# Optimization experiments

Measured on AMD Instinct MI355X. Metric: run time of the kernel, lower is better.

The kernel has to match this reference:

```python
import jax, jax.numpy as jnp
import numpy as np

N = 100000   # node_num
E = 1000000  # num edges
D = 256      # input_dim
H = 256      # hidden_dim


def setup_inputs() -> dict:
    key = jax.random.key(0)
    ks = jax.random.split(key, 6)
    x = jax.random.uniform(ks[0], (N, D), dtype=jnp.float32)  # nn.Parameter rand init
    edge_index = jax.random.randint(ks[1], (2, E), 0, N, dtype=jnp.int64)
    W1 = jax.random.normal(ks[2], (D, H), dtype=jnp.float32) * (1.0 / np.sqrt(D))
    b1 = jnp.zeros((H,), dtype=jnp.float32)
    W2 = jax.random.normal(ks[3], (H, H), dtype=jnp.float32) * (1.0 / np.sqrt(H))
    b2 = jnp.zeros((H,), dtype=jnp.float32)
    return {"edge_index": edge_index, "x": x, "W1": W1, "b1": b1, "W2": W2, "b2": b2}


def reference(edge_index, x, W1, b1, W2, b2):
    # GCNConv: add self-loops, symmetric normalization D^-1/2 (A+I) D^-1/2,
    # then (norm-weighted scatter-add of x@W) + bias, followed by ReLU.
    src, dst = edge_index[0], edge_index[1]
    loops = jnp.arange(N, dtype=src.dtype)
    s = jnp.concatenate([src, loops])          # [E+N] message sources
    d = jnp.concatenate([dst, loops])          # [E+N] message targets
    w = jnp.ones((E + N,), dtype=jnp.float32)  # edge_weight = 1 (incl. self-loops)
    deg = jax.ops.segment_sum(w, d, num_segments=N)
    dinv = jnp.where(deg > 0, jax.lax.rsqrt(deg), 0.0)
    norm = dinv[s] * w * dinv[d]               # [E+N]

    def layer(z, W, b):
        h = z @ W                                               # [N, H]
        agg = jax.ops.segment_sum(norm[:, None] * h[s], d, num_segments=N)
        return jax.nn.relu(agg + b)

    z = layer(x, W1, b1)
    z = layer(z, W2, b2)
    return z
```

## Files before the change

kernel.cpp:

```cpp
#include <hip/hip_runtime.h>
#include <stdint.h>

#define N_NODES 100000
#define N_EDGES 1000000
#define DIM 256
#define CAP 32

typedef __attribute__((ext_vector_type(8))) short short8;
typedef __attribute__((ext_vector_type(4))) float f32x4;
typedef __attribute__((ext_vector_type(4))) unsigned short u16x4;

__device__ inline float b2f(unsigned short u) {
    union { unsigned int i; float f; } v; v.i = ((unsigned int)u) << 16; return v.f;
}
__device__ inline unsigned short f2b(float f) {
    union { float f; unsigned int i; } v; v.f = f;
    unsigned int u = v.i;
    return (unsigned short)((u + 0x7FFFu + ((u >> 16) & 1u)) >> 16);
}


#define NB_FILL 245
#define NB_PACK 512
#define NB_CVT  25000

__global__ void k_pre(const int* __restrict__ src, const int* __restrict__ dst,
                      uint32_t* __restrict__ cnt, uint32_t* __restrict__ ovfCnt,
                      int* __restrict__ colM, uint32_t* __restrict__ ovf,
                      const float* __restrict__ W1, const float* __restrict__ W2,
                      unsigned short* __restrict__ Wt1, unsigned short* __restrict__ Wt2,
                      const float* __restrict__ x, unsigned short* __restrict__ xs) {
    int b = blockIdx.x, t = threadIdx.x;
    if (b < NB_FILL) {
        int e = b * 4096 + t;
        #pragma unroll
        for (int k = 0; k < 16; ++k, e += 256) {
            if (e < N_EDGES) {
                unsigned d = (unsigned)dst[e];
                unsigned s = (unsigned)src[e];
                if (d < N_NODES && s < N_NODES) {
                    uint32_t p = atomicAdd(&cnt[d], 1u);
                    if (p < CAP) colM[(size_t)d * CAP + p] = (int)s;
                    else {
                        uint32_t o = atomicAdd(ovfCnt, 1u);
                        if (o < (uint32_t)N_EDGES) { ovf[2 * o] = d; ovf[2 * o + 1] = s; }
                    }
                }
            }
        }
    } else if (b < NB_FILL + NB_PACK) {
        int n = b - NB_FILL;
        if (n < 256) Wt1[n * 256 + t] = f2b(W1[t * 256 + n]);
        else { n -= 256; Wt2[n * 256 + t] = f2b(W2[t * 256 + n]); }
    } else {
        int i = (b - (NB_FILL + NB_PACK)) * 256 + t;
        f32x4 v = __builtin_nontemporal_load((const f32x4*)x + i);
        u16x4 o;
        o.x = f2b(v.x); o.y = f2b(v.y); o.z = f2b(v.z); o.w = f2b(v.w);
        *((u16x4*)xs + i) = o;
    }
}

__global__ void k_wgt(const uint32_t* __restrict__ cnt, float* __restrict__ wgt) {
    int n = blockIdx.x * blockDim.x + threadIdx.x;
    if (n < N_NODES) wgt[n] = rsqrtf((float)(cnt[n] + 1u));
}

__global__ __launch_bounds__(256, 8) void k_gather(
        const unsigned short* __restrict__ rows, const uint32_t* __restrict__ cnt,
        const float* __restrict__ wgt,
        const uint32_t* __restrict__ ovfCnt, const int* __restrict__ colM,
        const uint32_t* __restrict__ ovf, unsigned short* __restrict__ out) {
    int wave = threadIdx.x >> 6, lane = threadIdx.x & 63;
    int node = blockIdx.x * 4 + wave;
    const u16x4* r4 = (const u16x4*)rows;

    uint32_t dgRaw = cnt[node];
    float    di    = wgt[node];
    uint32_t dg    = dgRaw < CAP ? dgRaw : CAP;
    uint32_t ovfN  = *ovfCnt;

    u16x4 sv = r4[(size_t)node * 64 + lane];
    float a[4];
    a[0] = di * b2f(sv.x); a[1] = di * b2f(sv.y);
    a[2] = di * b2f(sv.z); a[3] = di * b2f(sv.w);

    const int* cp = colM + (size_t)node * CAP;
    for (uint32_t j = 0; j < dg; j += 8) {
        int4 i0 = *(const int4*)(cp + j);
        int4 i1 = *(const int4*)(cp + j + 4);
        unsigned x0 = min((unsigned)i0.x, N_NODES - 1u);
        unsigned x1 = min((unsigned)i0.y, N_NODES - 1u);
        unsigned x2 = min((unsigned)i0.z, N_NODES - 1u);
        unsigned x3 = min((unsigned)i0.w, N_NODES - 1u);
        unsigned x4 = min((unsigned)i1.x, N_NODES - 1u);
        unsigned x5 = min((unsigned)i1.y, N_NODES - 1u);
        unsigned x6 = min((unsigned)i1.z, N_NODES - 1u);
        unsigned x7 = min((unsigned)i1.w, N_NODES - 1u);
        u16x4 r0 = r4[(size_t)x0 * 64 + lane];
        u16x4 r1 = r4[(size_t)x1 * 64 + lane];
        u16x4 r2 = r4[(size_t)x2 * 64 + lane];
        u16x4 r3 = r4[(size_t)x3 * 64 + lane];
        u16x4 r4v = r4[(size_t)x4 * 64 + lane];
        u16x4 r5 = r4[(size_t)x5 * 64 + lane];
        u16x4 r6 = r4[(size_t)x6 * 64 + lane];
        u16x4 r7 = r4[(size_t)x7 * 64 + lane];
        float w0 = (j + 0 < dg) ? wgt[x0] : 0.f;
        float w1 = (j + 1 < dg) ? wgt[x1] : 0.f;
        float w2 = (j + 2 < dg) ? wgt[x2] : 0.f;
        float w3 = (j + 3 < dg) ? wgt[x3] : 0.f;
        float w4 = (j + 4 < dg) ? wgt[x4] : 0.f;
        float w5 = (j + 5 < dg) ? wgt[x5] : 0.f;
        float w6 = (j + 6 < dg) ? wgt[x6] : 0.f;
        float w7 = (j + 7 < dg) ? wgt[x7] : 0.f;
        #pragma unroll
        for (int i = 0; i < 4; ++i) {
            float s = fmaf(w0, b2f(r0[i]), a[i]);
            s = fmaf(w1, b2f(r1[i]), s);
            s = fmaf(w2, b2f(r2[i]), s);
            s = fmaf(w3, b2f(r3[i]), s);
            s = fmaf(w4, b2f(r4v[i]), s);
            s = fmaf(w5, b2f(r5[i]), s);
            s = fmaf(w6, b2f(r6[i]), s);
            s = fmaf(w7, b2f(r7[i]), s);
            a[i] = s;
        }
    }

    if (ovfN) {
        for (uint32_t k = 0; k < ovfN; ++k) {
            uint32_t od = ovf[2 * k], os = ovf[2 * k + 1];
            if (od == (uint32_t)node) {
                float wv = wgt[os];
                u16x4 rv = r4[(size_t)os * 64 + lane];
                #pragma unroll
                for (int i = 0; i < 4; ++i) a[i] = fmaf(wv, b2f(rv[i]), a[i]);
            }
        }
    }

    u16x4 o;
    o.x = f2b(di * a[0]); o.y = f2b(di * a[1]);
    o.z = f2b(di * a[2]); o.w = f2b(di * a[3]);
    ((u16x4*)out)[(size_t)node * 64 + lane] = o;
}

__global__ __launch_bounds__(256, 4) void k_gemm(
        const unsigned short* __restrict__ A, const unsigned short* __restrict__ Wt,
        const float* __restrict__ bias,
        unsigned short* __restrict__ Cb, float* __restrict__ Cf) {
    __shared__ __align__(16) unsigned short As[64 * 256];

    int tid = threadIdx.x;
    int w = tid >> 6, lane = tid & 63;
    int rowBase = blockIdx.x * 64;

    #pragma unroll
    for (int i = 0; i < 8; ++i) {
        int c  = tid + i * 256;
        int r  = c >> 5;
        int kb = c & 31;
        int gr = rowBase + r;
        int4 v = {0, 0, 0, 0};
        if (gr < N_NODES) v = *(const int4*)(A + (size_t)gr * 256 + kb * 8);
        *(int4*)((char*)As + r * 512 + ((kb ^ (r & 7)) << 4)) = v;
    }
    __syncthreads();

    int m = lane & 15, quad = lane >> 4;

    f32x4 acc[4][4];
    #pragma unroll
    for (int mt = 0; mt < 4; ++mt)
        #pragma unroll
        for (int nt = 0; nt < 4; ++nt)
            acc[mt][nt] = (f32x4){0.f, 0.f, 0.f, 0.f};

    #pragma unroll
    for (int ks = 0; ks < 8; ++ks) {
        short8 wf[4], xf[4];
        #pragma unroll
        for (int nt = 0; nt < 4; ++nt)
            wf[nt] = *(const short8*)(Wt + (size_t)(w * 64 + nt * 16 + m) * 256 + ks * 32 + quad * 8);
        #pragma unroll
        for (int mt = 0; mt < 4; ++mt) {
            int rl = mt * 16 + m;
            int ch = (ks * 4 + quad) ^ (rl & 7);
            xf[mt] = *(const short8*)((const char*)As + rl * 512 + (ch << 4));
        }
        #pragma unroll
        for (int mt = 0; mt < 4; ++mt)
            #pragma unroll
            for (int nt = 0; nt < 4; ++nt)
                acc[mt][nt] = __builtin_amdgcn_mfma_f32_16x16x32_bf16(
                    wf[nt], xf[mt], acc[mt][nt], 0, 0, 0);
    }

    float4 bv[4];
    #pragma unroll
    for (int nt = 0; nt < 4; ++nt)
        bv[nt] = *(const float4*)(bias + w * 64 + nt * 16 + quad * 4);

    #pragma unroll
    for (int mt = 0; mt < 4; ++mt) {
        int node = rowBase + mt * 16 + m;
        if (node >= N_NODES) continue;
        if (Cf) {
            #pragma unroll
            for (int nt = 0; nt < 4; ++nt) {
                int c = w * 64 + nt * 16 + quad * 4;
                f32x4 v = acc[mt][nt];
                f32x4 o;
                o.x = fmaxf(v[0] + bv[nt].x, 0.f);
                o.y = fmaxf(v[1] + bv[nt].y, 0.f);
                o.z = fmaxf(v[2] + bv[nt].z, 0.f);
                o.w = fmaxf(v[3] + bv[nt].w, 0.f);
                __builtin_nontemporal_store(o, (f32x4*)(Cf + (size_t)node * 256 + c));
            }
        } else {
            #pragma unroll
            for (int nt = 0; nt < 4; ++nt) {
                int c = w * 64 + nt * 16 + quad * 4;
                f32x4 v = acc[mt][nt];
                u16x4 o;
                o.x = f2b(fmaxf(v[0] + bv[nt].x, 0.f));
                o.y = f2b(fmaxf(v[1] + bv[nt].y, 0.f));
                o.z = f2b(fmaxf(v[2] + bv[nt].z, 0.f));
                o.w = f2b(fmaxf(v[3] + bv[nt].w, 0.f));
                *(u16x4*)(Cb + (size_t)node * 256 + c) = o;
            }
        }
    }
}

extern "C" void kernel_launch(void* const* d_in, const int* in_sizes, int n_in,
                              void* d_out, int out_size, void* d_ws, size_t ws_size,
                              hipStream_t stream) {
    const int*   edge = (const int*)d_in[0];
    const float* x    = (const float*)d_in[1];
    const float* W1   = (const float*)d_in[2];
    const float* b1   = (const float*)d_in[3];
    const float* W2   = (const float*)d_in[4];
    const float* b2   = (const float*)d_in[5];
    float* out = (float*)d_out;

    char* ws = (char*)d_ws;
    uint32_t*       cnt    = (uint32_t*)(ws + 0);
    uint32_t*       ovfCnt = (uint32_t*)(ws + 400000);
    int*            colM   = (int*)     (ws + 400256);
    float*          wgt    = (float*)   (ws + 13200256);
    uint32_t*       ovf    = (uint32_t*)(ws + 13600256);
    unsigned short* Wt1    = (unsigned short*)(ws + 21600256);
    unsigned short* Wt2    = (unsigned short*)(ws + 21731328);
    unsigned short* xs     = (unsigned short*)(ws + 21862400);
    unsigned short* z1s    = (unsigned short*)(ws + 73062400ull);
    unsigned short* agg    = (unsigned short*)(ws + 124262400ull);

    const int* src = edge;
    const int* dst = edge + N_EDGES;

    hipMemsetAsync(ws, 0, 400256, stream);

    k_pre<<<NB_FILL + NB_PACK + NB_CVT, 256, 0, stream>>>(
        src, dst, cnt, ovfCnt, colM, ovf, W1, W2, Wt1, Wt2, x, xs);
    k_wgt<<<(N_NODES + 255) / 256, 256, 0, stream>>>(cnt, wgt);

    k_gather<<<N_NODES / 4, 256, 0, stream>>>(xs, cnt, wgt, ovfCnt, colM, ovf, agg);
    k_gemm<<<(N_NODES + 63) / 64, 256, 0, stream>>>(agg, Wt1, b1, z1s, nullptr);
    k_gather<<<N_NODES / 4, 256, 0, stream>>>(z1s, cnt, wgt, ovfCnt, colM, ovf, agg);
    k_gemm<<<(N_NODES + 63) / 64, 256, 0, stream>>>(agg, Wt2, b2, nullptr, out);
}
```

Before: 468.2 us.

## Fuse neighbor gather into GEMM kernel via shared-memory aggregation tile

```diff
diff --git a/kernel.cpp b/kernel.cpp
--- a/kernel.cpp
+++ b/kernel.cpp
@@ -66,87 +66,11 @@
     if (n < N_NODES) wgt[n] = rsqrtf((float)(cnt[n] + 1u));
 }
 
-__global__ __launch_bounds__(256, 8) void k_gather(
+__global__ __launch_bounds__(512, 8) void k_fused(
         const unsigned short* __restrict__ rows, const uint32_t* __restrict__ cnt,
         const float* __restrict__ wgt,
         const uint32_t* __restrict__ ovfCnt, const int* __restrict__ colM,
-        const uint32_t* __restrict__ ovf, unsigned short* __restrict__ out) {
-    int wave = threadIdx.x >> 6, lane = threadIdx.x & 63;
-    int node = blockIdx.x * 4 + wave;
-    const u16x4* r4 = (const u16x4*)rows;
-
-    uint32_t dgRaw = cnt[node];
-    float    di    = wgt[node];
-    uint32_t dg    = dgRaw < CAP ? dgRaw : CAP;
-    uint32_t ovfN  = *ovfCnt;
-
-    u16x4 sv = r4[(size_t)node * 64 + lane];
-    float a[4];
-    a[0] = di * b2f(sv.x); a[1] = di * b2f(sv.y);
-    a[2] = di * b2f(sv.z); a[3] = di * b2f(sv.w);
-
-    const int* cp = colM + (size_t)node * CAP;
-    for (uint32_t j = 0; j < dg; j += 8) {
-        int4 i0 = *(const int4*)(cp + j);
-        int4 i1 = *(const int4*)(cp + j + 4);
-        unsigned x0 = min((unsigned)i0.x, N_NODES - 1u);
-        unsigned x1 = min((unsigned)i0.y, N_NODES - 1u);
-        unsigned x2 = min((unsigned)i0.z, N_NODES - 1u);
-        unsigned x3 = min((unsigned)i0.w, N_NODES - 1u);
-        unsigned x4 = min((unsigned)i1.x, N_NODES - 1u);
-        unsigned x5 = min((unsigned)i1.y, N_NODES - 1u);
-        unsigned x6 = min((unsigned)i1.z, N_NODES - 1u);
-        unsigned x7 = min((unsigned)i1.w, N_NODES - 1u);
-        u16x4 r0 = r4[(size_t)x0 * 64 + lane];
-        u16x4 r1 = r4[(size_t)x1 * 64 + lane];
-        u16x4 r2 = r4[(size_t)x2 * 64 + lane];
-        u16x4 r3 = r4[(size_t)x3 * 64 + lane];
-        u16x4 r4v = r4[(size_t)x4 * 64 + lane];
-        u16x4 r5 = r4[(size_t)x5 * 64 + lane];
-        u16x4 r6 = r4[(size_t)x6 * 64 + lane];
-        u16x4 r7 = r4[(size_t)x7 * 64 + lane];
-        float w0 = (j + 0 < dg) ? wgt[x0] : 0.f;
-        float w1 = (j + 1 < dg) ? wgt[x1] : 0.f;
-        float w2 = (j + 2 < dg) ? wgt[x2] : 0.f;
-        float w3 = (j + 3 < dg) ? wgt[x3] : 0.f;
-        float w4 = (j + 4 < dg) ? wgt[x4] : 0.f;
-        float w5 = (j + 5 < dg) ? wgt[x5] : 0.f;
-        float w6 = (j + 6 < dg) ? wgt[x6] : 0.f;
-        float w7 = (j + 7 < dg) ? wgt[x7] : 0.f;
-        #pragma unroll
-        for (int i = 0; i < 4; ++i) {
-            float s = fmaf(w0, b2f(r0[i]), a[i]);
-            s = fmaf(w1, b2f(r1[i]), s);
-            s = fmaf(w2, b2f(r2[i]), s);
-            s = fmaf(w3, b2f(r3[i]), s);
-            s = fmaf(w4, b2f(r4v[i]), s);
-            s = fmaf(w5, b2f(r5[i]), s);
-            s = fmaf(w6, b2f(r6[i]), s);
-            s = fmaf(w7, b2f(r7[i]), s);
-            a[i] = s;
-        }
-    }
-
-    if (ovfN) {
-        for (uint32_t k = 0; k < ovfN; ++k) {
-            uint32_t od = ovf[2 * k], os = ovf[2 * k + 1];
-            if (od == (uint32_t)node) {
-                float wv = wgt[os];
-                u16x4 rv = r4[(size_t)os * 64 + lane];
-                #pragma unroll
-                for (int i = 0; i < 4; ++i) a[i] = fmaf(wv, b2f(rv[i]), a[i]);
-            }
-        }
-    }
-
-    u16x4 o;
-    o.x = f2b(di * a[0]); o.y = f2b(di * a[1]);
-    o.z = f2b(di * a[2]); o.w = f2b(di * a[3]);
-    ((u16x4*)out)[(size_t)node * 64 + lane] = o;
-}
-
-__global__ __launch_bounds__(256, 4) void k_gemm(
-        const unsigned short* __restrict__ A, const unsigned short* __restrict__ Wt,
+        const uint32_t* __restrict__ ovf, const unsigned short* __restrict__ Wt,
         const float* __restrict__ bias,
         unsigned short* __restrict__ Cb, float* __restrict__ Cf) {
     __shared__ __align__(16) unsigned short As[64 * 256];
@@ -154,81 +78,136 @@
     int tid = threadIdx.x;
     int w = tid >> 6, lane = tid & 63;
     int rowBase = blockIdx.x * 64;
-
+    uint32_t ovfN = *ovfCnt;
+    const u16x4* r4 = (const u16x4*)rows;
+
+    #pragma unroll 1
+    for (int s = 0; s < 8; ++s) {
+        int nl    = w * 8 + s;
+        int node  = rowBase + nl;
+        bool valid = node < N_NODES;
+        int nsafe = valid ? node : 0;
+
+        uint32_t dgRaw = cnt[nsafe];
+        float    di    = wgt[nsafe];
+        uint32_t dg    = valid ? (dgRaw < CAP ? dgRaw : CAP) : 0u;
+        float    wSelf = valid ? di : 0.f;
+
+        u16x4 sv = r4[(size_t)nsafe * 64 + lane];
+        float a[4];
+        a[0] = wSelf * b2f(sv.x); a[1] = wSelf * b2f(sv.y);
+        a[2] = wSelf * b2f(sv.z); a[3] = wSelf * b2f(sv.w);
+
+        const int* cp = colM + (size_t)nsafe * CAP;
+        for (uint32_t j = 0; j < dg; j += 8) {
+            int4 i0 = *(const int4*)(cp + j);
+            int4 i1 = *(const int4*)(cp + j + 4);
+            unsigned x0 = min((unsigned)i0.x, N_NODES - 1u);
+            unsigned x1 = min((unsigned)i0.y, N_NODES - 1u);
+            unsigned x2 = min((unsigned)i0.z, N_NODES - 1u);
+            unsigned x3 = min((unsigned)i0.w, N_NODES - 1u);
+            unsigned x4 = min((unsigned)i1.x, N_NODES - 1u);
+            unsigned x5 = min((unsigned)i1.y, N_NODES - 1u);
+            unsigned x6 = min((unsigned)i1.z, N_NODES - 1u);
+            unsigned x7 = min((unsigned)i1.w, N_NODES - 1u);
+            u16x4 r0 = r4[(size_t)x0 * 64 + lane];
+            u16x4 r1 = r4[(size_t)x1 * 64 + lane];
+            u16x4 r2 = r4[(size_t)x2 * 64 + lane];
+            u16x4 r3 = r4[(size_t)x3 * 64 + lane];
+            u16x4 r4v = r4[(size_t)x4 * 64 + lane];
+            u16x4 r5 = r4[(size_t)x5 * 64 + lane];
+            u16x4 r6 = r4[(size_t)x6 * 64 + lane];
+            u16x4 r7 = r4[(size_t)x7 * 64 + lane];
+            float w0 = (j + 0 < dg) ? wgt[x0] : 0.f;
+            float w1 = (j + 1 < dg) ? wgt[x1] : 0.f;
+            float w2 = (j + 2 < dg) ? wgt[x2] : 0.f;
+            float w3 = (j + 3 < dg) ? wgt[x3] : 0.f;
+            float w4 = (j + 4 < dg) ? wgt[x4] : 0.f;
+            float w5 = (j + 5 < dg) ? wgt[x5] : 0.f;
+            float w6 = (j + 6 < dg) ? wgt[x6] : 0.f;
+            float w7 = (j + 7 < dg) ? wgt[x7] : 0.f;
+            #pragma unroll
+            for (int i = 0; i < 4; ++i) {
+                float sacc = fmaf(w0, b2f(r0[i]), a[i]);
+                sacc = fmaf(w1, b2f(r1[i]), sacc);
+                sacc = fmaf(w2, b2f(r2[i]), sacc);
+                sacc = fmaf(w3, b2f(r3[i]), sacc);
+                sacc = fmaf(w4, b2f(r4v[i]), sacc);
+                sacc = fmaf(w5, b2f(r5[i]), sacc);
+                sacc = fmaf(w6, b2f(r6[i]), sacc);
+                sacc = fmaf(w7, b2f(r7[i]), sacc);
+                a[i] = sacc;
+            }
+        }
+
+        if (ovfN) {
+            for (uint32_t k = 0; k < ovfN; ++k) {
+                uint32_t od = ovf[2 * k], os = ovf[2 * k + 1];
+                if (valid && od == (uint32_t)node) {
+                    float wv = wgt[os];
+                    u16x4 rv = r4[(size_t)os * 64 + lane];
+                    #pragma unroll
+                    for (int i = 0; i < 4; ++i) a[i] = fmaf(wv, b2f(rv[i]), a[i]);
+                }
+            }
+        }
+
+        u16x4 o;
+        o.x = f2b(di * a[0]); o.y = f2b(di * a[1]);
+        o.z = f2b(di * a[2]); o.w = f2b(di * a[3]);
+        *(u16x4*)((char*)As + nl * 512 + ((((lane >> 1)) ^ (nl & 7)) << 4) + (lane & 1) * 8) = o;
+    }
+    __syncthreads();
+
+    int m = lane & 15, quad = lane >> 4;
+
+    f32x4 acc[4][2];
     #pragma unroll
-    for (int i = 0; i < 8; ++i) {
-        int c  = tid + i * 256;
-        int r  = c >> 5;
-        int kb = c & 31;
-        int gr = rowBase + r;
-        int4 v = {0, 0, 0, 0};
-        if (gr < N_NODES) v = *(const int4*)(A + (size_t)gr * 256 + kb * 8);
-        *(int4*)((char*)As + r * 512 + ((kb ^ (r & 7)) << 4)) = v;
-    }
-    __syncthreads();
-
-    int m = lane & 15, quad = lane >> 4;
-
-    f32x4 acc[4][4];
-    #pragma unroll
-    for (int mt = 0; mt < 4; ++mt)
-        #pragma unroll
-        for (int nt = 0; nt < 4; ++nt)
-            acc[mt][nt] = (f32x4){0.f, 0.f, 0.f, 0.f};
+    for (int mt = 0; mt < 4; ++mt) {
+        acc[mt][0] = (f32x4){0.f, 0.f, 0.f, 0.f};
+        acc[mt][1] = (f32x4){0.f, 0.f, 0.f, 0.f};
+    }
 
     #pragma unroll
     for (int ks = 0; ks < 8; ++ks) {
-        short8 wf[4], xf[4];
-        #pragma unroll
-        for (int nt = 0; nt < 4; ++nt)
-            wf[nt] = *(const short8*)(Wt + (size_t)(w * 64 + nt * 16 + m) * 256 + ks * 32 + quad * 8);
+        short8 wf0 = *(const short8*)(Wt + (size_t)(w * 32 + m)      * 256 + ks * 32 + quad * 8);
+        short8 wf1 = *(const short8*)(Wt + (size_t)(w * 32 + 16 + m) * 256 + ks * 32 + quad * 8);
         #pragma unroll
         for (int mt = 0; mt < 4; ++mt) {
             int rl = mt * 16 + m;
             int ch = (ks * 4 + quad) ^ (rl & 7);
-            xf[mt] = *(const short8*)((const char*)As + rl * 512 + (ch << 4));
-        }
-        #pragma unroll
-        for (int mt = 0; mt < 4; ++mt)
-            #pragma unroll
-            for (int nt = 0; nt < 4; ++nt)
-                acc[mt][nt] = __builtin_amdgcn_mfma_f32_16x16x32_bf16(
-                    wf[nt], xf[mt], acc[mt][nt], 0, 0, 0);
-    }
-
-    float4 bv[4];
-    #pragma unroll
-    for (int nt = 0; nt < 4; ++nt)
-        bv[nt] = *(const float4*)(bias + w * 64 + nt * 16 + quad * 4);
+            short8 xf = *(const short8*)((const char*)As + rl * 512 + (ch << 4));
+            acc[mt][0] = __builtin_amdgcn_mfma_f32_16x16x32_bf16(wf0, xf, acc[mt][0], 0, 0, 0);
+            acc[mt][1] = __builtin_amdgcn_mfma_f32_16x16x32_bf16(wf1, xf, acc[mt][1], 0, 0, 0);
+        }
+    }
+
+    float4 bv0 = *(const float4*)(bias + w * 32 + quad * 4);
+    float4 bv1 = *(const float4*)(bias + w * 32 + 16 + quad * 4);
 
     #pragma unroll
     for (int mt = 0; mt < 4; ++mt) {
         int node = rowBase + mt * 16 + m;
         if (node >= N_NODES) continue;
+        int c0 = w * 32 + quad * 4;
         if (Cf) {
-            #pragma unroll
-            for (int nt = 0; nt < 4; ++nt) {
-                int c = w * 64 + nt * 16 + quad * 4;
-                f32x4 v = acc[mt][nt];
-                f32x4 o;
-                o.x = fmaxf(v[0] + bv[nt].x, 0.f);
-                o.y = fmaxf(v[1] + bv[nt].y, 0.f);
-                o.z = fmaxf(v[2] + bv[nt].z, 0.f);
-                o.w = fmaxf(v[3] + bv[nt].w, 0.f);
-                __builtin_nontemporal_store(o, (f32x4*)(Cf + (size_t)node * 256 + c));
-            }
+            f32x4 v0 = acc[mt][0], v1 = acc[mt][1];
+            f32x4 o0, o1;
+            o0.x = fmaxf(v0[0] + bv0.x, 0.f); o0.y = fmaxf(v0[1] + bv0.y, 0.f);
+            o0.z = fmaxf(v0[2] + bv0.z, 0.f); o0.w = fmaxf(v0[3] + bv0.w, 0.f);
+            o1.x = fmaxf(v1[0] + bv1.x, 0.f); o1.y = fmaxf(v1[1] + bv1.y, 0.f);
+            o1.z = fmaxf(v1[2] + bv1.z, 0.f); o1.w = fmaxf(v1[3] + bv1.w, 0.f);
+            __builtin_nontemporal_store(o0, (f32x4*)(Cf + (size_t)node * 256 + c0));
+            __builtin_nontemporal_store(o1, (f32x4*)(Cf + (size_t)node * 256 + c0 + 16));
         } else {
-            #pragma unroll
-            for (int nt = 0; nt < 4; ++nt) {
-                int c = w * 64 + nt * 16 + quad * 4;
-                f32x4 v = acc[mt][nt];
-                u16x4 o;
-                o.x = f2b(fmaxf(v[0] + bv[nt].x, 0.f));
-                o.y = f2b(fmaxf(v[1] + bv[nt].y, 0.f));
-                o.z = f2b(fmaxf(v[2] + bv[nt].z, 0.f));
-                o.w = f2b(fmaxf(v[3] + bv[nt].w, 0.f));
-                *(u16x4*)(Cb + (size_t)node * 256 + c) = o;
-            }
+            f32x4 v0 = acc[mt][0], v1 = acc[mt][1];
+            u16x4 o0, o1;
+            o0.x = f2b(fmaxf(v0[0] + bv0.x, 0.f)); o0.y = f2b(fmaxf(v0[1] + bv0.y, 0.f));
+            o0.z = f2b(fmaxf(v0[2] + bv0.z, 0.f)); o0.w = f2b(fmaxf(v0[3] + bv0.w, 0.f));
+            o1.x = f2b(fmaxf(v1[0] + bv1.x, 0.f)); o1.y = f2b(fmaxf(v1[1] + bv1.y, 0.f));
+            o1.z = f2b(fmaxf(v1[2] + bv1.z, 0.f)); o1.w = f2b(fmaxf(v1[3] + bv1.w, 0.f));
+            *(u16x4*)(Cb + (size_t)node * 256 + c0)      = o0;
+            *(u16x4*)(Cb + (size_t)node * 256 + c0 + 16) = o1;
         }
     }
 }
@@ -254,7 +233,6 @@
     unsigned short* Wt2    = (unsigned short*)(ws + 21731328);
     unsigned short* xs     = (unsigned short*)(ws + 21862400);
     unsigned short* z1s    = (unsigned short*)(ws + 73062400ull);
-    unsigned short* agg    = (unsigned short*)(ws + 124262400ull);
 
     const int* src = edge;
     const int* dst = edge + N_EDGES;
@@ -265,8 +243,8 @@
         src, dst, cnt, ovfCnt, colM, ovf, W1, W2, Wt1, Wt2, x, xs);
     k_wgt<<<(N_NODES + 255) / 256, 256, 0, stream>>>(cnt, wgt);
 
-    k_gather<<<N_NODES / 4, 256, 0, stream>>>(xs, cnt, wgt, ovfCnt, colM, ovf, agg);
-    k_gemm<<<(N_NODES + 63) / 64, 256, 0, stream>>>(agg, Wt1, b1, z1s, nullptr);
-    k_gather<<<N_NODES / 4, 256, 0, stream>>>(z1s, cnt, wgt, ovfCnt, colM, ovf, agg);
-    k_gemm<<<(N_NODES + 63) / 64, 256, 0, stream>>>(agg, Wt2, b2, nullptr, out);
-}
+    k_fused<<<(N_NODES + 63) / 64, 512, 0, stream>>>(
+        xs, cnt, wgt, ovfCnt, colM, ovf, Wt1, b1, z1s, nullptr);
+    k_fused<<<(N_NODES + 63) / 64, 512, 0, stream>>>(
+        z1s, cnt, wgt, ovfCnt, colM, ovf, Wt2, b2, nullptr, out);
+}
```

After: 454.6 us. 2.9% less time.
